# Kernel tuning notes

Measured on AMD Instinct MI355X. Metric: run time of the kernel, lower is better.

## Reference

```python
import jax, jax.numpy as jnp
import numpy as np

SHAPES = ((96, 144), (48, 72), (24, 36), (12, 18))
BS, EMBED = 2, 256
HEADS, LEVELS, POINTS = 8, 4, 4
NEMBED = EMBED // HEADS
LEN_V = sum(h * w for h, w in SHAPES)
LEN_Q = LEN_V  # encoder self-attention: every pixel is a query


def _pos_grid_init():
    # Faithful re-implementation of MultiScaleDeformableAttention.pos_grid_init
    thetas = jnp.arange(HEADS, dtype=jnp.float32) * (2.0 * np.pi / HEADS)
    g = jnp.stack([jnp.cos(thetas), jnp.sin(thetas)], -1)
    g = g / jnp.max(jnp.abs(g), axis=-1, keepdims=True)
    g = jnp.tile(g.reshape(HEADS, 1, 1, 2), (1, LEVELS, POINTS, 1))
    scale = (jnp.arange(POINTS, dtype=jnp.float32) + 1.0)[None, None, :, None]
    return g * scale  # [HEADS, LEVELS, POINTS, 2]


def setup_inputs() -> dict:
    ks = jax.random.split(jax.random.key(0), 7)
    return {
        'query': jax.random.normal(ks[0], (BS, LEN_Q, EMBED), jnp.float32),
        'ref_points': jax.random.uniform(ks[1], (BS, LEN_Q, LEVELS, 2), jnp.float32),
        'value': jax.random.normal(ks[2], (BS, LEN_V, EMBED), jnp.float32),
        'pad_mask': jnp.ones((BS, LEN_V), dtype=bool),
        'value_proj_kernel': jax.random.normal(ks[3], (EMBED, HEADS, NEMBED), jnp.float32) * 0.05,
        'value_proj_bias': jnp.zeros((HEADS, NEMBED), jnp.float32),
        'sampling_offsets_kernel': jax.random.normal(ks[4], (EMBED, HEADS, LEVELS, POINTS, 2), jnp.float32) * 0.01,
        'sampling_offsets_bias': _pos_grid_init(),
        'attn_kernel': jax.random.normal(ks[5], (EMBED, HEADS, LEVELS * POINTS), jnp.float32) * 0.02,
        'attn_bias': jnp.zeros((HEADS, LEVELS * POINTS), jnp.float32),
        'out_kernel': jax.random.normal(ks[6], (HEADS, NEMBED, EMBED), jnp.float32) * 0.05,
        'out_bias': jnp.zeros((EMBED,), jnp.float32),
        'train': 0,
    }


def _bilinear(im, grid, w, h):
    """Batched 2D bilinear interpolation, zero outside the image.

    im:   [B, h*w, e] flattened feature map
    grid: [B, N, 2] normalized coords (pixel centers at (x+0.5)/w, (y+0.5)/h)
    Returns [B, N, e]. Identical math to the original gather-based kernel:
    out-of-bounds corner weights are zeroed, so zero-padding the image by 1
    reproduces the 'empty'-pad + masked-weight scheme exactly.
    """
    B, _, e = im.shape
    imp = jnp.pad(im.reshape(B, h, w, e), ((0, 0), (1, 1), (1, 1), (0, 0)))
    imp = imp.reshape(B, (h + 2) * (w + 2), e)
    x = grid[..., 0] * w - 0.5
    y = grid[..., 1] * h - 0.5
    x0 = jnp.floor(x).astype(jnp.int32)
    y0 = jnp.floor(y).astype(jnp.int32)
    x1 = x0 + 1
    y1 = y0 + 1

    def gather(yy, xx):
        idx = jnp.clip(yy + 1, 0, h + 1) * (w + 2) + jnp.clip(xx + 1, 0, w + 1)
        return jnp.take_along_axis(imp, idx[..., None], axis=1)  # [B, N, e]

    x0f, y0f = x0.astype(x.dtype), y0.astype(y.dtype)
    x1f, y1f = x1.astype(x.dtype), y1.astype(y.dtype)
    inx0 = (x0 >= 0) & (x0 <= w - 1)
    inx1 = (x1 >= 0) & (x1 <= w - 1)
    iny0 = (y0 >= 0) & (y0 <= h - 1)
    iny1 = (y1 >= 0) & (y1 <= h - 1)
    wa = jnp.where(inx0 & iny0, (x1f - x) * (y1f - y), 0.0)
    wb = jnp.where(inx0 & iny1, (x1f - x) * (y - y0f), 0.0)
    wc = jnp.where(inx1 & iny0, (x - x0f) * (y1f - y), 0.0)
    wd = jnp.where(inx1 & iny1, (x - x0f) * (y - y0f), 0.0)
    return (gather(y0, x0) * wa[..., None] + gather(y1, x0) * wb[..., None]
            + gather(y0, x1) * wc[..., None] + gather(y1, x1) * wd[..., None])


def _forward(query, ref_points, value, pad_mask, vpk, vpb, sok, sob, ak, ab, okern, obias):
    bs, len_q, _ = query.shape
    len_v = value.shape[1]
    # value projection + pad masking -> [bs*H, len_v, nembed]
    v = jnp.einsum('bve,ehd->bvhd', value, vpk) + vpb
    v = jnp.where(pad_mask[..., None, None], v, 0)
    v = v.transpose(0, 2, 1, 3).reshape(bs * HEADS, len_v, NEMBED)
    # sampling locations (ref_dim == 2 branch) -> [bs*H, L, P*len_q, 2]
    off = jnp.einsum('bqe,ehlpc->bqhlpc', query, sok) + sob
    offset_norm = jnp.array([[w, h] for h, w in SHAPES], dtype=query.dtype)  # [L, 2]
    loc = ref_points[:, :, None, :, None, :] + off / offset_norm[None, None, None, :, None, :]
    loc = loc.transpose(0, 2, 3, 4, 1, 5).reshape(bs * HEADS, LEVELS, POINTS * len_q, 2)
    # attention weights (softmax over L*P) -> [bs*H, len_q, L*P]
    aw = jnp.einsum('bqe,ehm->bqhm', query, ak) + ab
    aw = jax.nn.softmax(aw, axis=-1)
    aw = aw.transpose(0, 2, 1, 3).reshape(bs * HEADS, len_q, LEVELS * POINTS)
    # per-level bilinear sampling, concatenated level-major over (level, point)
    starts = np.cumsum([0] + [h * w for h, w in SHAPES])
    sampled = []
    for li, (h, w) in enumerate(SHAPES):
        vl = v[:, starts[li]:starts[li + 1], :]
        s = _bilinear(vl, loc[:, li], w, h)  # [bs*H, P*len_q, nembed]
        sampled.append(s.reshape(bs * HEADS, POINTS, len_q, NEMBED))
    sampled = jnp.concatenate(sampled, axis=1)  # [bs*H, L*P, len_q, nembed]
    x = jnp.einsum('blqe,bql->bqe', sampled, aw)
    x = x.reshape(bs, HEADS, len_q, NEMBED)
    # output projection: DenseGeneral over (heads, nembed)
    return jnp.einsum('bhqe,hed->bqd', x, okern) + obias


def reference(query, ref_points, value, pad_mask, value_proj_kernel, value_proj_bias,
              sampling_offsets_kernel, sampling_offsets_bias, attn_kernel, attn_bias,
              out_kernel, out_bias, train):
    del train  # eval mode (no remat); math is identical
    return _forward(query, ref_points, value, pad_mask, value_proj_kernel, value_proj_bias,
                    sampling_offsets_kernel, sampling_offsets_bias, attn_kernel, attn_bias,
                    out_kernel, out_bias)
```

## Files before the change

### kernel.cpp

```cpp
#include <hip/hip_runtime.h>
#include <hip/hip_fp16.h>
#include <math.h>

#define LEN 18360
#define M_ROWS (2 * LEN)
#define NTASK (16 * LEN)

typedef unsigned short u16;
typedef __attribute__((ext_vector_type(8))) short bf16x8;
typedef __attribute__((ext_vector_type(4))) float f32x4;

__device__ __forceinline__ u16 f2bf(float f) {
  unsigned u = __float_as_uint(f);
  return (u16)((u + 0x7fffu + ((u >> 16) & 1u)) >> 16);
}

__global__ __launch_bounds__(256) void gemm_mfma_k(
    const u16* __restrict__ A0, const u16* __restrict__ Bt0,
    const float* __restrict__ bias0, void* __restrict__ C0, int N0, int nt0,
    int mode0, int split, const u16* __restrict__ A1,
    const u16* __restrict__ Bt1, const float* __restrict__ bias1,
    void* __restrict__ C1, int N1, int nt1, int mode1) {
  int bid = (int)blockIdx.x;
  const u16* A;
  const u16* Bt;
  const float* bias;
  void* Cv;
  int N, nt, mode;
  if (bid < split) {
    A = A0; Bt = Bt0; bias = bias0; Cv = C0; N = N0; nt = nt0; mode = mode0;
  } else {
    bid -= split;
    A = A1; Bt = Bt1; bias = bias1; Cv = C1; N = N1; nt = nt1; mode = mode1;
  }
  const int n0 = (bid % nt) << 7;
  const int m0 = (bid / nt) << 7;

  const int tid = threadIdx.x;
  const int w = tid >> 6;
  const int lane = tid & 63;
  const int wm = w & 1, wn = w >> 1;
  const int mr = lane & 15;
  const int kq = (lane >> 4) * 8;

  const u16* arow[4];
  const u16* brow[4];
#pragma unroll
  for (int i = 0; i < 4; i++) {
    const int ga = min(m0 + wm * 64 + i * 16 + mr, M_ROWS - 1);
    arow[i] = A + (size_t)ga * 256 + kq;
    const int gb = n0 + wn * 64 + i * 16 + mr;
    brow[i] = Bt + (size_t)gb * 256 + kq;
  }

  f32x4 acc[4][4];
#pragma unroll
  for (int i = 0; i < 4; i++)
#pragma unroll
    for (int j = 0; j < 4; j++) acc[i][j] = (f32x4){0.f, 0.f, 0.f, 0.f};

#pragma unroll 2
  for (int k0 = 0; k0 < 256; k0 += 32) {
    bf16x8 af[4], bf[4];
#pragma unroll
    for (int i = 0; i < 4; i++) af[i] = *(const bf16x8*)(arow[i] + k0);
#pragma unroll
    for (int j = 0; j < 4; j++) bf[j] = *(const bf16x8*)(brow[j] + k0);
#pragma unroll
    for (int i = 0; i < 4; i++)
#pragma unroll
      for (int j = 0; j < 4; j++)
        acc[i][j] = __builtin_amdgcn_mfma_f32_16x16x32_bf16(bf[j], af[i],
                                                            acc[i][j], 0, 0, 0);
  }

#pragma unroll
  for (int i = 0; i < 4; i++) {
    const int row = m0 + wm * 64 + i * 16 + mr;
    if (row >= M_ROWS) continue;
#pragma unroll
    for (int j = 0; j < 4; j++) {
      const int col = n0 + wn * 64 + j * 16 + (lane >> 4) * 4;
      const float4 b4 = *(const float4*)(bias + col);
      float4 o;
      o.x = acc[i][j][0] + b4.x;
      o.y = acc[i][j][1] + b4.y;
      o.z = acc[i][j][2] + b4.z;
      o.w = acc[i][j][3] + b4.w;
      if (mode == 0) {
        *(float4*)((float*)Cv + (size_t)row * N + col) = o;
      } else if (mode == 1) {
        const int b = row >= LEN;
        const int lv = row - b * LEN;
        const int h = col >> 5, d = col & 31;
        __half2 ha = __floats2half2_rn(o.x, o.y);
        __half2 hb = __floats2half2_rn(o.z, o.w);
        uint2 p;
        p.x = *(unsigned*)&ha;
        p.y = *(unsigned*)&hb;
        *(uint2*)((u16*)Cv + ((size_t)((b * 8 + h) * LEN + lv)) * 32 + d) = p;
      } else {
        uint2 p;
        p.x = (unsigned)f2bf(o.x) | ((unsigned)f2bf(o.y) << 16);
        p.y = (unsigned)f2bf(o.z) | ((unsigned)f2bf(o.w) << 16);
        *(uint2*)((u16*)Cv + (size_t)row * N + col) = p;
      }
    }
  }
}

__global__ __launch_bounds__(256) void prep_k(
    const float* __restrict__ q, const float* __restrict__ v,
    u16* __restrict__ qb, u16* __restrict__ vb, const float* __restrict__ vpk,
    const float* __restrict__ sok, const float* __restrict__ ak,
    const float* __restrict__ ok, const float* __restrict__ sob,
    const float* __restrict__ ab, u16* __restrict__ vpk_t,
    u16* __restrict__ sa_t, u16* __restrict__ ok_t,
    float* __restrict__ bias_cat) {
  __shared__ float tile[32][33];
  const int bid = blockIdx.x, tid = threadIdx.x;
  if (bid < 9180) {
    const size_t i = ((size_t)bid * 256 + tid) * 4;
    float4 a = *(const float4*)(q + i);
    uint2 p;
    p.x = (unsigned)f2bf(a.x) | ((unsigned)f2bf(a.y) << 16);
    p.y = (unsigned)f2bf(a.z) | ((unsigned)f2bf(a.w) << 16);
    *(uint2*)&qb[i] = p;
    float4 c = *(const float4*)(v + i);
    p.x = (unsigned)f2bf(c.x) | ((unsigned)f2bf(c.y) << 16);
    p.y = (unsigned)f2bf(c.z) | ((unsigned)f2bf(c.w) << 16);
    *(uint2*)&vb[i] = p;
    return;
  }
  int tb = bid - 9180;
  if (tb < 224) {
    const float* src;
    u16* dst;
    int ncols, lt;
    if (tb < 64) { src = vpk; dst = vpk_t; ncols = 256; lt = tb; }
    else if (tb < 128) { src = sok; dst = sa_t; ncols = 256; lt = tb - 64; }
    else if (tb < 160) { src = ak; dst = sa_t + 65536; ncols = 128; lt = tb - 128; }
    else { src = ok; dst = ok_t; ncols = 256; lt = tb - 160; }
    const int ntx = ncols >> 5;
    const int k0 = (lt / ntx) << 5, c0 = (lt % ntx) << 5;
    const int r = tid >> 5, cc = tid & 31;
#pragma unroll
    for (int p = 0; p < 4; p++)
      tile[r + 8 * p][cc] = src[(size_t)(k0 + r + 8 * p) * ncols + c0 + cc];
    __syncthreads();
#pragma unroll
    for (int p = 0; p < 4; p++)
      dst[(size_t)(c0 + r + 8 * p) * 256 + k0 + cc] = f2bf(tile[cc][r + 8 * p]);
    return;
  }
  for (int i = tid; i < 384; i += 256)
    bias_cat[i] = (i < 256) ? sob[i] : ab[i - 256];
}

__global__ __launch_bounds__(256) void sampler_k(
    const u16* __restrict__ v,
    const u16* __restrict__ offaw,
    const float* __restrict__ refp,
    u16* __restrict__ xb)
{
  __shared__ int2 meta[16 * 66];
  const int tid = threadIdx.x;

  const int cW[4] = {144, 72, 36, 18};
  const int cH[4] = {96, 48, 24, 12};
  const int cS[4] = {0, 13824, 17280, 18144};

  {
    const int T = tid >> 4;
    const int s = tid & 15;
    const int l = s >> 2;

    const int task = (blockIdx.x << 4) + T;
    const int q = task % LEN;
    const int bh = task / LEN;
    const int h = bh & 7;
    const int b = bh >> 3;
    const size_t qrow = (size_t)(b * LEN + q);
    const u16* rowp = offaw + qrow * 384;

    const float logit = __uint_as_float((unsigned)rowp[256 + h * 16 + s] << 16);
    float mx = logit;
#pragma unroll
    for (int m = 1; m < 16; m <<= 1) mx = fmaxf(mx, __shfl_xor(mx, m, 16));
    const float e = __expf(logit - mx);
    float ssum = e;
#pragma unroll
    for (int m = 1; m < 16; m <<= 1) ssum += __shfl_xor(ssum, m, 16);
    const float wsm = e / ssum;

    const int W = cW[l], H = cH[l], ST = cS[l];
    const float2 rp = ((const float2*)(refp + qrow * 8))[l];
    const unsigned upair = ((const unsigned*)(rowp + h * 32))[s];
    const float ox = __uint_as_float(upair << 16);
    const float oy = __uint_as_float(upair & 0xffff0000u);
    const float X = rp.x * (float)W + ox - 0.5f;
    const float Y = rp.y * (float)H + oy - 0.5f;
    const float fx = floorf(X), fy = floorf(Y);
    const int x0 = (int)fx, y0 = (int)fy;
    const float dx = X - fx, dy = Y - fy;
    const float ux = 1.f - dx, uy = 1.f - dy;
    const bool bx0 = (unsigned)x0 < (unsigned)W;
    const bool bx1 = (unsigned)(x0 + 1) < (unsigned)W;
    const bool by0 = (unsigned)y0 < (unsigned)H;
    const bool by1 = (unsigned)(y0 + 1) < (unsigned)H;
    const int xc0 = min(max(x0, 0), W - 1);
    const int xc1 = min(max(x0 + 1, 0), W - 1);
    const int yc0 = min(max(y0, 0), H - 1);
    const int yc1 = min(max(y0 + 1, 0), H - 1);
    const float w00 = (bx0 & by0) ? wsm * ux * uy : 0.f;
    const float w10 = (bx1 & by0) ? wsm * dx * uy : 0.f;
    const float w01 = (bx0 & by1) ? wsm * ux * dy : 0.f;
    const float w11 = (bx1 & by1) ? wsm * dx * dy : 0.f;

    int2* mp = &meta[T * 66 + s * 4];
    mp[0] = make_int2((ST + yc0 * W + xc0) << 6, __float_as_int(w00));
    mp[1] = make_int2((ST + yc0 * W + xc1) << 6, __float_as_int(w10));
    mp[2] = make_int2((ST + yc1 * W + xc0) << 6, __float_as_int(w01));
    mp[3] = make_int2((ST + yc1 * W + xc1) << 6, __float_as_int(w11));
  }
  __syncthreads();

  const int wv = tid >> 6;
  const int lane = tid & 63;
  const int T = wv * 4 + (lane >> 4);
  const int c = (lane >> 2) & 3;
  const int dq = lane & 3;

  const int task = (blockIdx.x << 4) + T;
  const int q = task % LEN;
  const int bh = task / LEN;
  const int h = bh & 7;
  const int b = bh >> 3;
  const size_t qrow = (size_t)(b * LEN + q);
  const char* vb = (const char*)v + (size_t)bh * LEN * 64;

  float acc[8];
#pragma unroll
  for (int j = 0; j < 8; j++) acc[j] = 0.f;

#pragma unroll
  for (int s = 0; s < 16; s++) {
    const int2 m2 = meta[T * 66 + s * 4 + c];
    const float wgt = __int_as_float(m2.y);
    const uint4 pv =
        *(const uint4*)(vb + (size_t)(unsigned)m2.x + (dq << 4));
    const __half2* h2 = (const __half2*)&pv;
#pragma unroll
    for (int j = 0; j < 4; j++) {
      const float2 f = __half22float2(h2[j]);
      acc[2 * j] = fmaf(wgt, f.x, acc[2 * j]);
      acc[2 * j + 1] = fmaf(wgt, f.y, acc[2 * j + 1]);
    }
  }
#pragma unroll
  for (int m = 4; m <= 8; m <<= 1)
#pragma unroll
    for (int j = 0; j < 8; j++) acc[j] += __shfl_xor(acc[j], m, 64);

  if (c == 0) {
    uint4 p;
    p.x = (unsigned)f2bf(acc[0]) | ((unsigned)f2bf(acc[1]) << 16);
    p.y = (unsigned)f2bf(acc[2]) | ((unsigned)f2bf(acc[3]) << 16);
    p.z = (unsigned)f2bf(acc[4]) | ((unsigned)f2bf(acc[5]) << 16);
    p.w = (unsigned)f2bf(acc[6]) | ((unsigned)f2bf(acc[7]) << 16);
    *(uint4*)&xb[qrow * 256 + h * 32 + (dq << 3)] = p;
  }
}

extern "C" void kernel_launch(void* const* d_in, const int* in_sizes, int n_in,
                              void* d_out, int out_size, void* d_ws,
                              size_t ws_size, hipStream_t stream) {
  (void)in_sizes; (void)n_in; (void)out_size; (void)ws_size;

  const float* query = (const float*)d_in[0];
  const float* refp = (const float*)d_in[1];
  const float* value = (const float*)d_in[2];
  const float* vpk = (const float*)d_in[4];
  const float* vpb = (const float*)d_in[5];
  const float* sok = (const float*)d_in[6];
  const float* sob = (const float*)d_in[7];
  const float* ak = (const float*)d_in[8];
  const float* ab = (const float*)d_in[9];
  const float* okern = (const float*)d_in[10];
  const float* obias = (const float*)d_in[11];

  char* p = (char*)d_ws;
  u16* v_ws = (u16*)p;   p += (size_t)M_ROWS * 256 * 2;
  u16* offaw = (u16*)p;  p += (size_t)M_ROWS * 384 * 2;
  u16* qbf = (u16*)p;    p += (size_t)M_ROWS * 256 * 2;
  u16* vbf = (u16*)p;    p += (size_t)M_ROWS * 256 * 2;
  u16* vpk_t = (u16*)p;  p += 65536 * 2;
  u16* sa_t = (u16*)p;   p += 98304 * 2;
  u16* ok_t = (u16*)p;   p += 65536 * 2;
  float* bias_cat = (float*)p;
  u16* x_b = qbf;

  const dim3 blk(256);
  const int mt = (M_ROWS + 127) / 128;

  prep_k<<<dim3(9405), blk, 0, stream>>>(query, value, qbf, vbf, vpk, sok, ak,
                                         okern, sob, ab, vpk_t, sa_t, ok_t,
                                         bias_cat);
  gemm_mfma_k<<<dim3(2 * mt + 3 * mt), blk, 0, stream>>>(
      vbf, vpk_t, vpb, v_ws, 256, 2, 1, 2 * mt,
      qbf, sa_t, bias_cat, offaw, 384, 3, 2);
  sampler_k<<<dim3(NTASK / 16), blk, 0, stream>>>(v_ws, offaw, refp, x_b);
  gemm_mfma_k<<<dim3(2 * mt), blk, 0, stream>>>(
      x_b, ok_t, obias, (float*)d_out, 256, 2, 0, 2 * mt,
      x_b, ok_t, obias, (float*)d_out, 256, 2, 0);
}
```

Baseline: 276.1 us.

## Keep full-K B tile resident in registers and stream 256-row A strips

Restructures the MFMA GEMM so each block holds a 64-column slice of the weight matrix over all of K (8x4 bf16x8 fragments) in registers. The block then loops over four 64-row sub-strips of A, with each wave computing 16 rows, and bias loads are hoisted out of the loop. This avoids reloading the small weight matrix per K step and raises the launch bound to 2 blocks per CU. The cost is fewer accumulators per wave (4 tiles instead of 16), less A reuse across N, more blocks, and high register pressure from the resident B fragments.

```diff
diff --git a/kernel.cpp b/kernel.cpp
--- a/kernel.cpp
+++ b/kernel.cpp
@@ -15,7 +15,7 @@
   return (u16)((u + 0x7fffu + ((u >> 16) & 1u)) >> 16);
 }
 
-__global__ __launch_bounds__(256) void gemm_mfma_k(
+__global__ __launch_bounds__(256, 2) void gemm_rs_k(
     const u16* __restrict__ A0, const u16* __restrict__ Bt0,
     const float* __restrict__ bias0, void* __restrict__ C0, int N0, int nt0,
     int mode0, int split, const u16* __restrict__ A1,
@@ -33,77 +33,75 @@
     bid -= split;
     A = A1; Bt = Bt1; bias = bias1; Cv = C1; N = N1; nt = nt1; mode = mode1;
   }
-  const int n0 = (bid % nt) << 7;
-  const int m0 = (bid / nt) << 7;
+  const int n0 = (bid % nt) << 6;
+  const int mb = bid / nt;
 
   const int tid = threadIdx.x;
   const int w = tid >> 6;
   const int lane = tid & 63;
-  const int wm = w & 1, wn = w >> 1;
   const int mr = lane & 15;
   const int kq = (lane >> 4) * 8;
 
-  const u16* arow[4];
-  const u16* brow[4];
-#pragma unroll
-  for (int i = 0; i < 4; i++) {
-    const int ga = min(m0 + wm * 64 + i * 16 + mr, M_ROWS - 1);
-    arow[i] = A + (size_t)ga * 256 + kq;
-    const int gb = n0 + wn * 64 + i * 16 + mr;
-    brow[i] = Bt + (size_t)gb * 256 + kq;
-  }
-
-  f32x4 acc[4][4];
-#pragma unroll
-  for (int i = 0; i < 4; i++)
-#pragma unroll
-    for (int j = 0; j < 4; j++) acc[i][j] = (f32x4){0.f, 0.f, 0.f, 0.f};
-
-#pragma unroll 2
-  for (int k0 = 0; k0 < 256; k0 += 32) {
-    bf16x8 af[4], bf[4];
-#pragma unroll
-    for (int i = 0; i < 4; i++) af[i] = *(const bf16x8*)(arow[i] + k0);
-#pragma unroll
-    for (int j = 0; j < 4; j++) bf[j] = *(const bf16x8*)(brow[j] + k0);
-#pragma unroll
-    for (int i = 0; i < 4; i++)
+  bf16x8 bf[8][4];
+#pragma unroll
+  for (int kk = 0; kk < 8; kk++)
+#pragma unroll
+    for (int j = 0; j < 4; j++)
+      bf[kk][j] =
+          *(const bf16x8*)(Bt + (size_t)(n0 + j * 16 + mr) * 256 + kk * 32 + kq);
+
+  float4 b4[4];
+#pragma unroll
+  for (int j = 0; j < 4; j++)
+    b4[j] = *(const float4*)(bias + n0 + j * 16 + (lane >> 4) * 4);
+
+#pragma unroll
+  for (int s = 0; s < 4; s++) {
+    const int rowb = mb * 256 + s * 64 + w * 16;
+    const int ga = min(rowb + mr, M_ROWS - 1);
+    const u16* ap = A + (size_t)ga * 256 + kq;
+    bf16x8 af[8];
+#pragma unroll
+    for (int kk = 0; kk < 8; kk++) af[kk] = *(const bf16x8*)(ap + kk * 32);
+
+    f32x4 acc[4];
+#pragma unroll
+    for (int j = 0; j < 4; j++) acc[j] = (f32x4){0.f, 0.f, 0.f, 0.f};
+#pragma unroll
+    for (int kk = 0; kk < 8; kk++)
 #pragma unroll
       for (int j = 0; j < 4; j++)
-        acc[i][j] = __builtin_amdgcn_mfma_f32_16x16x32_bf16(bf[j], af[i],
-                                                            acc[i][j], 0, 0, 0);
-  }
-
-#pragma unroll
-  for (int i = 0; i < 4; i++) {
-    const int row = m0 + wm * 64 + i * 16 + mr;
-    if (row >= M_ROWS) continue;
-#pragma unroll
-    for (int j = 0; j < 4; j++) {
-      const int col = n0 + wn * 64 + j * 16 + (lane >> 4) * 4;
-      const float4 b4 = *(const float4*)(bias + col);
-      float4 o;
-      o.x = acc[i][j][0] + b4.x;
-      o.y = acc[i][j][1] + b4.y;
-      o.z = acc[i][j][2] + b4.z;
-      o.w = acc[i][j][3] + b4.w;
-      if (mode == 0) {
-        *(float4*)((float*)Cv + (size_t)row * N + col) = o;
-      } else if (mode == 1) {
-        const int b = row >= LEN;
-        const int lv = row - b * LEN;
-        const int h = col >> 5, d = col & 31;
-        __half2 ha = __floats2half2_rn(o.x, o.y);
-        __half2 hb = __floats2half2_rn(o.z, o.w);
-        uint2 p;
-        p.x = *(unsigned*)&ha;
-        p.y = *(unsigned*)&hb;
-        *(uint2*)((u16*)Cv + ((size_t)((b * 8 + h) * LEN + lv)) * 32 + d) = p;
-      } else {
-        uint2 p;
-        p.x = (unsigned)f2bf(o.x) | ((unsigned)f2bf(o.y) << 16);
-        p.y = (unsigned)f2bf(o.z) | ((unsigned)f2bf(o.w) << 16);
-        *(uint2*)((u16*)Cv + (size_t)row * N + col) = p;
+        acc[j] = __builtin_amdgcn_mfma_f32_16x16x32_bf16(bf[kk][j], af[kk],
+                                                         acc[j], 0, 0, 0);
+
+    const int row = rowb + mr;
+    if (row < M_ROWS) {
+#pragma unroll
+      for (int j = 0; j < 4; j++) {
+        const int col = n0 + j * 16 + (lane >> 4) * 4;
+        float4 o;
+        o.x = acc[j][0] + b4[j].x;
+        o.y = acc[j][1] + b4[j].y;
+        o.z = acc[j][2] + b4[j].z;
+        o.w = acc[j][3] + b4[j].w;
+        if (mode == 0) {
+          *(float4*)((float*)Cv + (size_t)row * N + col) = o;
+        } else if (mode == 1) {
+          const int b = row >= LEN;
+          const int lv = row - b * LEN;
+          const int h = col >> 5, d = col & 31;
+          __half2 ha = __floats2half2_rn(o.x, o.y);
+          __half2 hb = __floats2half2_rn(o.z, o.w);
+          uint2 p;
+          p.x = *(unsigned*)&ha;
+          p.y = *(unsigned*)&hb;
+          *(uint2*)((u16*)Cv + ((size_t)((b * 8 + h) * LEN + lv)) * 32 + d) = p;
+        } else {
+          uint2 p;
+          p.x = (unsigned)f2bf(o.x) | ((unsigned)f2bf(o.y) << 16);
+          p.y = (unsigned)f2bf(o.z) | ((unsigned)f2bf(o.w) << 16);
+          *(uint2*)((u16*)Cv + (size_t)row * N + col) = p;
+        }
       }
     }
   }
@@ -301,16 +299,16 @@
   u16* x_b = qbf;
 
   const dim3 blk(256);
-  const int mt = (M_ROWS + 127) / 128;
+  const int mgrp = (M_ROWS + 255) / 256;
 
   prep_k<<<dim3(9405), blk, 0, stream>>>(query, value, qbf, vbf, vpk, sok, ak,
                                          okern, sob, ab, vpk_t, sa_t, ok_t,
                                          bias_cat);
-  gemm_mfma_k<<<dim3(2 * mt + 3 * mt), blk, 0, stream>>>(
-      vbf, vpk_t, vpb, v_ws, 256, 2, 1, 2 * mt,
-      qbf, sa_t, bias_cat, offaw, 384, 3, 2);
+  gemm_rs_k<<<dim3(mgrp * 4 + mgrp * 6), blk, 0, stream>>>(
+      vbf, vpk_t, vpb, v_ws, 256, 4, 1, mgrp * 4,
+      qbf, sa_t, bias_cat, offaw, 384, 6, 2);
   sampler_k<<<dim3(NTASK / 16), blk, 0, stream>>>(v_ws, offaw, refp, x_b);
-  gemm_mfma_k<<<dim3(2 * mt), blk, 0, stream>>>(
-      x_b, ok_t, obias, (float*)d_out, 256, 2, 0, 2 * mt,
-      x_b, ok_t, obias, (float*)d_out, 256, 2, 0);
-}
+  gemm_rs_k<<<dim3(mgrp * 4), blk, 0, stream>>>(
+      x_b, ok_t, obias, (float*)d_out, 256, 4, 0, mgrp * 4,
+      x_b, ok_t, obias, (float*)d_out, 256, 4, 0);
+}
```

Measured after the change: 281.8 us. +2.1%, slower.
